# Optimization experiments

Measured on AMD Instinct MI355X. Metric: run time of the kernel, lower is better.

## Reference

```python
import jax, jax.numpy as jnp
import numpy as np

P, G, F, H = 128, 256, 1024, 512
EPS = 1e-5

def _bn(x, g, b, m, v):
    # eval-mode BatchNorm1d over last dim
    return (x - m) / jnp.sqrt(v + EPS) * g + b

def _lrelu(x):
    return jnp.where(x > 0, x, 0.1 * x)

def setup_inputs():
    key = jax.random.key(0)
    ks = iter(jax.random.split(key, 64))
    rn = lambda s, sc=1.0: jax.random.normal(next(ks), s, dtype=jnp.float32) * sc
    ru = lambda s: jax.random.uniform(next(ks), s, dtype=jnp.float32) + 0.5
    return {
        "f_p": rn((P, F)), "f_g": rn((G, F)),
        "bn_g": ru((F,)), "bn_b": rn((F,), 0.1), "bn_m": rn((F,), 0.1), "bn_v": ru((F,)),
        "rf_W1": rn((F, F), 0.02), "rf_b1": rn((F,), 0.01),
        "rf1_g": ru((F,)), "rf1_b": rn((F,), 0.1), "rf1_m": rn((F,), 0.1), "rf1_v": ru((F,)),
        "rf_W2": rn((F, F), 0.02), "rf_b2": rn((F,), 0.01),
        "rf2_g": ru((F,)), "rf2_b": rn((F,), 0.1), "rf2_m": rn((F,), 0.1), "rf2_v": ru((F,)),
        "sfc_W": rn((F, H), 0.02), "sfc_b": rn((H,), 0.01),
        "sbn_g": ru((H,)), "sbn_b": rn((H,), 0.1), "sbn_m": rn((H,), 0.1), "sbn_v": ru((H,)),
        "scl_W": rn((H, 1), 0.001), "scl_b": rn((1,), 0.001),
        "ffc_W": rn((F, H), 0.02), "ffc_b": rn((H,), 0.01),
        "fbn_g": ru((H,)), "fbn_b": rn((H,), 0.1), "fbn_m": rn((H,), 0.1), "fbn_v": ru((H,)),
        "cls_W": rn((H, 1), 0.001), "cls_b": rn((1,), 0.001),
    }

def reference(f_p, f_g, bn_g, bn_b, bn_m, bn_v,
              rf_W1, rf_b1, rf1_g, rf1_b, rf1_m, rf1_v,
              rf_W2, rf_b2, rf2_g, rf2_b, rf2_m, rf2_v,
              sfc_W, sfc_b, sbn_g, sbn_b, sbn_m, sbn_v, scl_W, scl_b,
              ffc_W, ffc_b, fbn_g, fbn_b, fbn_m, fbn_v, cls_W, cls_b):
    # Siamese difference feature for every probe-gallery pair: d [P,G,F]
    d = _bn((f_p[:, None, :] - f_g[None, :, :]) ** 2, bn_g, bn_b, bn_m, bn_v)
    h = _lrelu(_bn(d @ rf_W1 + rf_b1, rf1_g, rf1_b, rf1_m, rf1_v))
    t = _lrelu(_bn(h @ rf_W2 + rf_b2, rf2_g, rf2_b, rf2_m, rf2_v))
    # Gallery-gallery scalar affinities via Siamese FcBlock + ClassBlock: w [G,G]
    dg = _bn((f_g[:, None, :] - f_g[None, :, :]) ** 2, bn_g, bn_b, bn_m, bn_v)
    hg = _lrelu(_bn(dg @ sfc_W + sfc_b, sbn_g, sbn_b, sbn_m, sbn_v))
    w = (hg @ scl_W + scl_b)[..., 0]
    # Graph diffusion over the gallery axis: d_new = t @ w  [P,G,F]
    d_new = jnp.einsum('pgf,gh->phf', t, w)
    # Per-pair FC + classifier -> scalar score per (probe, gallery) pair
    feat = _lrelu(_bn(d_new @ ffc_W + ffc_b, fbn_g, fbn_b, fbn_m, fbn_v))
    result = (feat @ cls_W + cls_b)[..., 0]
    return result
```

## Files before the change

kernel.cpp:

```cpp
#include <hip/hip_runtime.h>


typedef __bf16 bf16;
typedef __attribute__((ext_vector_type(8))) __bf16 bf16x8;
typedef __attribute__((ext_vector_type(4))) float f32x4;

#define EPSV 1e-5f

__device__ __forceinline__ void async_load16(const bf16* g, bf16* l) {
    __builtin_amdgcn_global_load_lds(
        (const __attribute__((address_space(1))) void*)g,
        (__attribute__((address_space(3))) void*)l, 16, 0, 0);
}

__global__ __launch_bounds__(256) void prep_kernel(
    const float* __restrict__ g, const float* __restrict__ b,
    const float* __restrict__ m, const float* __restrict__ v,
    const float* __restrict__ bias, float* __restrict__ scale,
    float* __restrict__ offset, int n)
{
    int i = blockIdx.x * 256 + threadIdx.x;
    if (i >= n) return;
    float s = g[i] / sqrtf(v[i] + EPSV);
    float o = b[i] - m[i] * s;
    if (bias) o += bias[i] * s;
    scale[i] = s;
    offset[i] = o;
}

__global__ __launch_bounds__(256) void wtrans_kernel(
    const float* __restrict__ in, bf16* __restrict__ out, int K, int N)
{
    int k = blockIdx.x * 256 + threadIdx.x;
    int n = blockIdx.y;
    out[(size_t)n * K + k] = (bf16)in[(size_t)k * N + n];
}

__global__ __launch_bounds__(256) void wconv_kernel(
    const float* __restrict__ w_acc, const float* __restrict__ sclb,
    bf16* __restrict__ wT)
{
    int tid = blockIdx.x * 256 + threadIdx.x;
    int g2 = tid >> 8, g1 = tid & 255;
    int idx = ((g1 >> 4) <= (g2 >> 4)) ? (g1 * 256 + g2) : (g2 * 256 + g1);
    wT[tid] = (bf16)(w_acc[idx] + sclb[0]);
}

__global__ __launch_bounds__(256) void finout_kernel(
    const float* __restrict__ acc, const float* __restrict__ clsb,
    float* __restrict__ out)
{
    int i = blockIdx.x * 256 + threadIdx.x;
    out[i] = acc[i] + clsb[0];
}

__global__ __launch_bounds__(512) void gemm256(
    const bf16* __restrict__ A,
    const float* __restrict__ pairX, const float* __restrict__ pairY,
    const float* __restrict__ ps, const float* __restrict__ po,
    const bf16* __restrict__ BT,
    bf16* __restrict__ C,
    int K, int N, int rowOff,
    long long batchA, long long batchB, long long batchC,
    const float* __restrict__ scale, const float* __restrict__ offset,
    int lrelu,
    const float* __restrict__ fuseW, float* __restrict__ facc,
    long long faccStride)
{
    __shared__ bf16 As[256 * 64];
    __shared__ bf16 Bs[256 * 64];
    const int tid  = threadIdx.x;
    const int lane = tid & 63;
    const int wave = tid >> 6;
    const int wrow = wave >> 2, wcol = wave & 3;
    const int row0 = blockIdx.y * 256;
    const int col0 = blockIdx.x * 256;
    const int q = lane >> 4, l16 = lane & 15;
    const int z = blockIdx.z;

    const bf16* Ap = A + (size_t)z * (size_t)batchA;
    const bf16* Bp = BT + (size_t)z * (size_t)batchB;

    f32x4 acc[8][4];
#pragma unroll
    for (int mi = 0; mi < 8; ++mi)
#pragma unroll
        for (int ni = 0; ni < 4; ++ni)
#pragma unroll
            for (int e = 0; e < 4; ++e) acc[mi][ni][e] = 0.f;

    for (int kk = 0; kk < K; kk += 64) {
        if (pairX) {
#pragma unroll
            for (int t = 0; t < 4; ++t) {
                int c = tid + t * 512;
                int r = c >> 3, ch = c & 7;
                int gr = rowOff + row0 + r;
                const float* xp = pairX + (size_t)(gr >> 8) * K + kk + ch * 8;
                const float* yp = pairY + (size_t)(gr & 255) * K + kk + ch * 8;
                f32x4 x0 = *(const f32x4*)xp, x1 = *(const f32x4*)(xp + 4);
                f32x4 y0 = *(const f32x4*)yp, y1 = *(const f32x4*)(yp + 4);
                f32x4 sa = *(const f32x4*)(ps + kk + ch * 8);
                f32x4 sb = *(const f32x4*)(ps + kk + ch * 8 + 4);
                f32x4 oa = *(const f32x4*)(po + kk + ch * 8);
                f32x4 ob = *(const f32x4*)(po + kk + ch * 8 + 4);
                bf16x8 dv;
#pragma unroll
                for (int j = 0; j < 4; ++j) {
                    float d0 = x0[j] - y0[j];
                    float d1 = x1[j] - y1[j];
                    dv[j]     = (bf16)(d0 * d0 * sa[j] + oa[j]);
                    dv[j + 4] = (bf16)(d1 * d1 * sb[j] + ob[j]);
                }
                *(bf16x8*)&As[r * 64 + ((ch ^ (r & 7)) * 8)] = dv;
            }
        } else {
#pragma unroll
            for (int t = 0; t < 4; ++t) {
                int idx = t * 512 + tid;
                int r = idx >> 3, sch = idx & 7;
                int gch = sch ^ (r & 7);
                async_load16(Ap + (size_t)(row0 + r) * K + kk + gch * 8,
                             &As[idx * 8]);
            }
        }
#pragma unroll
        for (int t = 0; t < 4; ++t) {
            int idx = t * 512 + tid;
            int r = idx >> 3, sch = idx & 7;
            int gch = sch ^ (r & 7);
            async_load16(Bp + (size_t)(col0 + r) * K + kk + gch * 8,
                         &Bs[idx * 8]);
        }
        __syncthreads();

#pragma unroll
        for (int s = 0; s < 2; ++s) {
            bf16x8 af[8], bfr[4];
#pragma unroll
            for (int mi = 0; mi < 8; ++mi) {
                int r = wrow * 128 + mi * 16 + l16;
                af[mi] = *(const bf16x8*)&As[r * 64 + (((s * 4 + q) ^ (r & 7)) * 8)];
            }
#pragma unroll
            for (int ni = 0; ni < 4; ++ni) {
                int rc = wcol * 64 + ni * 16 + l16;
                bfr[ni] = *(const bf16x8*)&Bs[rc * 64 + (((s * 4 + q) ^ (rc & 7)) * 8)];
            }
#pragma unroll
            for (int mi = 0; mi < 8; ++mi)
#pragma unroll
                for (int ni = 0; ni < 4; ++ni)
                    acc[mi][ni] = __builtin_amdgcn_mfma_f32_16x16x32_bf16(
                        af[mi], bfr[ni], acc[mi][ni], 0, 0, 0);
        }
        __syncthreads();
    }

    if (fuseW) {
#pragma unroll
        for (int mi = 0; mi < 8; ++mi)
#pragma unroll
            for (int i = 0; i < 4; ++i) {
                float rs = 0.f;
#pragma unroll
                for (int ni = 0; ni < 4; ++ni) {
                    int cc = col0 + wcol * 64 + ni * 16 + l16;
                    float val = acc[mi][ni][i] * scale[cc] + offset[cc];
                    val = val > 0.f ? val : 0.1f * val;
                    rs += val * fuseW[cc];
                }
                rs += __shfl_xor(rs, 1, 64);
                rs += __shfl_xor(rs, 2, 64);
                rs += __shfl_xor(rs, 4, 64);
                rs += __shfl_xor(rs, 8, 64);
                if (l16 == 0) {
                    int r = row0 + wrow * 128 + mi * 16 + q * 4 + i;
                    atomicAdd(facc + (size_t)z * faccStride + r, rs);
                }
            }
        return;
    }
    bf16* Cp = C + (size_t)z * (size_t)batchC;
#pragma unroll
    for (int mi = 0; mi < 8; ++mi)
#pragma unroll
        for (int ni = 0; ni < 4; ++ni)
#pragma unroll
            for (int i = 0; i < 4; ++i) {
                int r = row0 + wrow * 128 + mi * 16 + q * 4 + i;
                int cc = col0 + wcol * 64 + ni * 16 + l16;
                float val = acc[mi][ni][i];
                if (scale) val = val * scale[cc] + offset[cc];
                if (lrelu) val = val > 0.f ? val : 0.1f * val;
                Cp[(size_t)r * N + cc] = (bf16)val;
            }
}

__global__ __launch_bounds__(512) void gemm_aff(
    const float* __restrict__ pairX,
    const float* __restrict__ ps, const float* __restrict__ po,
    const bf16* __restrict__ BT,
    int K,
    const float* __restrict__ scale, const float* __restrict__ offset,
    const float* __restrict__ sclW, float* __restrict__ w_acc)
{
    __shared__ bf16 As[256 * 64];
    __shared__ bf16 Bs[128 * 64];
    const int tid  = threadIdx.x;
    const int lane = tid & 63;
    const int wave = tid >> 6;
    const int wrow = wave >> 1, wcol = wave & 1;
    const int q = lane >> 4, l16 = lane & 15;
    const int col0 = blockIdx.x * 128;

    int ta = 0, rem = blockIdx.y;
    while (rem >= 16 - ta) { rem -= 16 - ta; ++ta; }
    const int tb = ta + rem;

    f32x4 acc[4][4];
#pragma unroll
    for (int mi = 0; mi < 4; ++mi)
#pragma unroll
        for (int ni = 0; ni < 4; ++ni)
#pragma unroll
            for (int e = 0; e < 4; ++e) acc[mi][ni][e] = 0.f;

    for (int kk = 0; kk < K; kk += 64) {
#pragma unroll
        for (int t = 0; t < 4; ++t) {
            int c = tid + t * 512;
            int r = c >> 3, ch = c & 7;
            int g1 = ta * 16 + (r >> 4), g2 = tb * 16 + (r & 15);
            const float* xp = pairX + (size_t)g1 * K + kk + ch * 8;
            const float* yp = pairX + (size_t)g2 * K + kk + ch * 8;
            f32x4 x0 = *(const f32x4*)xp, x1 = *(const f32x4*)(xp + 4);
            f32x4 y0 = *(const f32x4*)yp, y1 = *(const f32x4*)(yp + 4);
            f32x4 sa = *(const f32x4*)(ps + kk + ch * 8);
            f32x4 sb = *(const f32x4*)(ps + kk + ch * 8 + 4);
            f32x4 oa = *(const f32x4*)(po + kk + ch * 8);
            f32x4 ob = *(const f32x4*)(po + kk + ch * 8 + 4);
            bf16x8 dv;
#pragma unroll
            for (int j = 0; j < 4; ++j) {
                float d0 = x0[j] - y0[j];
                float d1 = x1[j] - y1[j];
                dv[j]     = (bf16)(d0 * d0 * sa[j] + oa[j]);
                dv[j + 4] = (bf16)(d1 * d1 * sb[j] + ob[j]);
            }
            *(bf16x8*)&As[r * 64 + ((ch ^ (r & 7)) * 8)] = dv;
        }
#pragma unroll
        for (int t = 0; t < 2; ++t) {
            int idx = t * 512 + tid;
            int r = idx >> 3, sch = idx & 7;
            int gch = sch ^ (r & 7);
            async_load16(BT + (size_t)(col0 + r) * K + kk + gch * 8,
                         &Bs[idx * 8]);
        }
        __syncthreads();

#pragma unroll
        for (int s = 0; s < 2; ++s) {
            bf16x8 af[4], bfr[4];
#pragma unroll
            for (int mi = 0; mi < 4; ++mi) {
                int r = wrow * 64 + mi * 16 + l16;
                af[mi] = *(const bf16x8*)&As[r * 64 + (((s * 4 + q) ^ (r & 7)) * 8)];
            }
#pragma unroll
            for (int ni = 0; ni < 4; ++ni) {
                int rc = wcol * 64 + ni * 16 + l16;
                bfr[ni] = *(const bf16x8*)&Bs[rc * 64 + (((s * 4 + q) ^ (rc & 7)) * 8)];
            }
#pragma unroll
            for (int mi = 0; mi < 4; ++mi)
#pragma unroll
                for (int ni = 0; ni < 4; ++ni)
                    acc[mi][ni] = __builtin_amdgcn_mfma_f32_16x16x32_bf16(
                        af[mi], bfr[ni], acc[mi][ni], 0, 0, 0);
        }
        __syncthreads();
    }

#pragma unroll
    for (int mi = 0; mi < 4; ++mi)
#pragma unroll
        for (int i = 0; i < 4; ++i) {
            float rs = 0.f;
#pragma unroll
            for (int ni = 0; ni < 4; ++ni) {
                int cc = col0 + wcol * 64 + ni * 16 + l16;
                float val = acc[mi][ni][i] * scale[cc] + offset[cc];
                val = val > 0.f ? val : 0.1f * val;
                rs += val * sclW[cc];
            }
            rs += __shfl_xor(rs, 1, 64);
            rs += __shfl_xor(rs, 2, 64);
            rs += __shfl_xor(rs, 4, 64);
            rs += __shfl_xor(rs, 8, 64);
            if (l16 == 0) {
                int r = wrow * 64 + mi * 16 + q * 4 + i;
                int g1 = ta * 16 + (r >> 4), g2 = tb * 16 + (r & 15);
                atomicAdd(w_acc + g1 * 256 + g2, rs);
            }
        }
}

extern "C" void kernel_launch(void* const* d_in, const int* in_sizes, int n_in,
                              void* d_out, int out_size, void* d_ws, size_t ws_size,
                              hipStream_t stream)
{
    const float* f_p   = (const float*)d_in[0];
    const float* f_g   = (const float*)d_in[1];
    const float* bn_g  = (const float*)d_in[2];
    const float* bn_b  = (const float*)d_in[3];
    const float* bn_m  = (const float*)d_in[4];
    const float* bn_v  = (const float*)d_in[5];
    const float* rf_W1 = (const float*)d_in[6];
    const float* rf_b1 = (const float*)d_in[7];
    const float* rf1_g = (const float*)d_in[8];
    const float* rf1_b = (const float*)d_in[9];
    const float* rf1_m = (const float*)d_in[10];
    const float* rf1_v = (const float*)d_in[11];
    const float* rf_W2 = (const float*)d_in[12];
    const float* rf_b2 = (const float*)d_in[13];
    const float* rf2_g = (const float*)d_in[14];
    const float* rf2_b = (const float*)d_in[15];
    const float* rf2_m = (const float*)d_in[16];
    const float* rf2_v = (const float*)d_in[17];
    const float* sfc_W = (const float*)d_in[18];
    const float* sfc_b = (const float*)d_in[19];
    const float* sbn_g = (const float*)d_in[20];
    const float* sbn_b = (const float*)d_in[21];
    const float* sbn_m = (const float*)d_in[22];
    const float* sbn_v = (const float*)d_in[23];
    const float* scl_W = (const float*)d_in[24];
    const float* scl_b = (const float*)d_in[25];
    const float* ffc_W = (const float*)d_in[26];
    const float* ffc_b = (const float*)d_in[27];
    const float* fbn_g = (const float*)d_in[28];
    const float* fbn_b = (const float*)d_in[29];
    const float* fbn_m = (const float*)d_in[30];
    const float* fbn_v = (const float*)d_in[31];
    const float* cls_W = (const float*)d_in[32];
    const float* cls_b = (const float*)d_in[33];

    const size_t MB = 1ull << 20;
    char* ws = (char*)d_ws;
    float* SC      = (float*)(ws);
    float *s0 = SC,        *o0 = SC + 1024;
    float *s1 = SC + 2048, *o1 = SC + 3072;
    float *s2 = SC + 4096, *o2 = SC + 5120;
    float *s3 = SC + 6144, *o3 = SC + 6656;
    float *s4 = SC + 7168, *o4 = SC + 7680;
    float* w_acc   = (float*)(ws + 65536);
    float* out_acc = (float*)(ws + 327680);
    bf16* wT       = (bf16*)(ws + 458752);
    bf16* W1T      = (bf16*)(ws + 1 * MB);
    bf16* W2T      = (bf16*)(ws + 3 * MB);
    bf16* sfcT     = (bf16*)(ws + 5 * MB);
    bf16* ffcT     = (bf16*)(ws + 6 * MB);

    int nc;
    if      (ws_size >= 170 * MB) nc = 1;
    else if (ws_size >= 90 * MB)  nc = 2;
    else                          nc = 4;
    const int pc = 128 / nc;
    const int R  = pc * 256;
    const size_t hbytes = (size_t)R * 1024 * 2;
    bf16* bufA = (bf16*)(ws + 8 * MB);
    bf16* bufB = (bf16*)(ws + 8 * MB + hbytes);
    bf16* bufC = (bf16*)(ws + 8 * MB + 2 * hbytes);

    prep_kernel<<<dim3(4), 256, 0, stream>>>(bn_g, bn_b, bn_m, bn_v, nullptr, s0, o0, 1024);
    prep_kernel<<<dim3(4), 256, 0, stream>>>(rf1_g, rf1_b, rf1_m, rf1_v, rf_b1, s1, o1, 1024);
    prep_kernel<<<dim3(4), 256, 0, stream>>>(rf2_g, rf2_b, rf2_m, rf2_v, rf_b2, s2, o2, 1024);
    prep_kernel<<<dim3(2), 256, 0, stream>>>(sbn_g, sbn_b, sbn_m, sbn_v, sfc_b, s3, o3, 512);
    prep_kernel<<<dim3(2), 256, 0, stream>>>(fbn_g, fbn_b, fbn_m, fbn_v, ffc_b, s4, o4, 512);

    wtrans_kernel<<<dim3(4, 1024), 256, 0, stream>>>(rf_W1, W1T, 1024, 1024);
    wtrans_kernel<<<dim3(4, 1024), 256, 0, stream>>>(rf_W2, W2T, 1024, 1024);
    wtrans_kernel<<<dim3(4, 512), 256, 0, stream>>>(sfc_W, sfcT, 1024, 512);
    wtrans_kernel<<<dim3(4, 512), 256, 0, stream>>>(ffc_W, ffcT, 1024, 512);

    hipMemsetAsync(ws + 65536, 0, 393216, stream);

    gemm_aff<<<dim3(4, 136), 512, 0, stream>>>(
        f_g, s0, o0, sfcT, 1024, s3, o3, scl_W, w_acc);
    wconv_kernel<<<dim3(256), 256, 0, stream>>>(w_acc, scl_b, wT);

    for (int ci = 0; ci < nc; ++ci) {
        gemm256<<<dim3(4, R / 256), 512, 0, stream>>>(
            nullptr, f_p, f_g, s0, o0, W1T, bufA, 1024, 1024, ci * R,
            0, 0, 0, s1, o1, 1, nullptr, nullptr, 0);
        gemm256<<<dim3(4, R / 256), 512, 0, stream>>>(
            bufA, nullptr, nullptr, nullptr, nullptr, W2T, bufB, 1024, 1024, 0,
            0, 0, 0, s2, o2, 1, nullptr, nullptr, 0);
        gemm256<<<dim3(1, 2, pc), 512, 0, stream>>>(
            ffcT, nullptr, nullptr, nullptr, nullptr, bufB, bufC, 1024, 256, 0,
            0, (long long)256 * 1024, (long long)512 * 256,
            nullptr, nullptr, 0, nullptr, nullptr, 0);
        gemm256<<<dim3(2, 1, pc), 512, 0, stream>>>(
            wT, nullptr, nullptr, nullptr, nullptr, bufC, nullptr, 256, 512, 0,
            0, (long long)512 * 256, 0,
            s4, o4, 1, cls_W, out_acc + (size_t)ci * pc * 256, 256);
    }
    finout_kernel<<<dim3(128), 256, 0, stream>>>(out_acc, cls_b, (float*)d_out);
}
```

Measured before the change: 566.7 us.

## Fuse gallery affinity GEMM into second ReFine GEMM launch as extra blocks

Adds a combined kernel whose first blocks compute the second ReFine linear layer and whose remaining blocks compute the gallery-gallery affinity GEMM with its fused classifier reduction. This lets the small affinity work fill the GPU alongside the large GEMM instead of running as a separate serial launch beforehand. The combined path is used only when the whole pair set fits in one chunk. Mixing heterogeneous blocks may unbalance scheduling, and the shared memory footprint is sized for the larger tile.

```diff
diff --git a/kernel.cpp b/kernel.cpp
--- a/kernel.cpp
+++ b/kernel.cpp
@@ -52,6 +52,214 @@
 {
     int i = blockIdx.x * 256 + threadIdx.x;
     out[i] = acc[i] + clsb[0];
+}
+
+__device__ __forceinline__ void dev_gemm256_plain(
+    bf16* As, bf16* Bs,
+    const bf16* __restrict__ A, const bf16* __restrict__ BT,
+    bf16* __restrict__ C, int K, int N, int row0, int col0,
+    const float* __restrict__ scale, const float* __restrict__ offset,
+    int lrelu)
+{
+    const int tid  = threadIdx.x;
+    const int lane = tid & 63;
+    const int wave = tid >> 6;
+    const int wrow = wave >> 2, wcol = wave & 3;
+    const int q = lane >> 4, l16 = lane & 15;
+
+    f32x4 acc[8][4];
+#pragma unroll
+    for (int mi = 0; mi < 8; ++mi)
+#pragma unroll
+        for (int ni = 0; ni < 4; ++ni)
+#pragma unroll
+            for (int e = 0; e < 4; ++e) acc[mi][ni][e] = 0.f;
+
+    for (int kk = 0; kk < K; kk += 64) {
+#pragma unroll
+        for (int t = 0; t < 4; ++t) {
+            int idx = t * 512 + tid;
+            int r = idx >> 3, sch = idx & 7;
+            int gch = sch ^ (r & 7);
+            async_load16(A + (size_t)(row0 + r) * K + kk + gch * 8,
+                         &As[idx * 8]);
+        }
+#pragma unroll
+        for (int t = 0; t < 4; ++t) {
+            int idx = t * 512 + tid;
+            int r = idx >> 3, sch = idx & 7;
+            int gch = sch ^ (r & 7);
+            async_load16(BT + (size_t)(col0 + r) * K + kk + gch * 8,
+                         &Bs[idx * 8]);
+        }
+        __syncthreads();
+#pragma unroll
+        for (int s = 0; s < 2; ++s) {
+            bf16x8 af[8], bfr[4];
+#pragma unroll
+            for (int mi = 0; mi < 8; ++mi) {
+                int r = wrow * 128 + mi * 16 + l16;
+                af[mi] = *(const bf16x8*)&As[r * 64 + (((s * 4 + q) ^ (r & 7)) * 8)];
+            }
+#pragma unroll
+            for (int ni = 0; ni < 4; ++ni) {
+                int rc = wcol * 64 + ni * 16 + l16;
+                bfr[ni] = *(const bf16x8*)&Bs[rc * 64 + (((s * 4 + q) ^ (rc & 7)) * 8)];
+            }
+#pragma unroll
+            for (int mi = 0; mi < 8; ++mi)
+#pragma unroll
+                for (int ni = 0; ni < 4; ++ni)
+                    acc[mi][ni] = __builtin_amdgcn_mfma_f32_16x16x32_bf16(
+                        af[mi], bfr[ni], acc[mi][ni], 0, 0, 0);
+        }
+        __syncthreads();
+    }
+
+#pragma unroll
+    for (int mi = 0; mi < 8; ++mi)
+#pragma unroll
+        for (int ni = 0; ni < 4; ++ni)
+#pragma unroll
+            for (int i = 0; i < 4; ++i) {
+                int r = row0 + wrow * 128 + mi * 16 + q * 4 + i;
+                int cc = col0 + wcol * 64 + ni * 16 + l16;
+                float val = acc[mi][ni][i];
+                if (scale) val = val * scale[cc] + offset[cc];
+                if (lrelu) val = val > 0.f ? val : 0.1f * val;
+                C[(size_t)r * N + cc] = (bf16)val;
+            }
+}
+
+__device__ __forceinline__ void dev_aff(
+    bf16* As, bf16* Bs,
+    const float* __restrict__ pairX,
+    const float* __restrict__ ps, const float* __restrict__ po,
+    const bf16* __restrict__ BT, int K, int col0, int triIdx,
+    const float* __restrict__ scale, const float* __restrict__ offset,
+    const float* __restrict__ sclW, float* __restrict__ w_acc)
+{
+    const int tid  = threadIdx.x;
+    const int lane = tid & 63;
+    const int wave = tid >> 6;
+    const int wrow = wave >> 1, wcol = wave & 1;
+    const int q = lane >> 4, l16 = lane & 15;
+
+    int ta = 0, rem = triIdx;
+    while (rem >= 16 - ta) { rem -= 16 - ta; ++ta; }
+    const int tb = ta + rem;
+
+    f32x4 acc[4][4];
+#pragma unroll
+    for (int mi = 0; mi < 4; ++mi)
+#pragma unroll
+        for (int ni = 0; ni < 4; ++ni)
+#pragma unroll
+            for (int e = 0; e < 4; ++e) acc[mi][ni][e] = 0.f;
+
+    for (int kk = 0; kk < K; kk += 64) {
+#pragma unroll
+        for (int t = 0; t < 4; ++t) {
+            int c = tid + t * 512;
+            int r = c >> 3, ch = c & 7;
+            int g1 = ta * 16 + (r >> 4), g2 = tb * 16 + (r & 15);
+            const float* xp = pairX + (size_t)g1 * K + kk + ch * 8;
+            const float* yp = pairX + (size_t)g2 * K + kk + ch * 8;
+            f32x4 x0 = *(const f32x4*)xp, x1 = *(const f32x4*)(xp + 4);
+            f32x4 y0 = *(const f32x4*)yp, y1 = *(const f32x4*)(yp + 4);
+            f32x4 sa = *(const f32x4*)(ps + kk + ch * 8);
+            f32x4 sb = *(const f32x4*)(ps + kk + ch * 8 + 4);
+            f32x4 oa = *(const f32x4*)(po + kk + ch * 8);
+            f32x4 ob = *(const f32x4*)(po + kk + ch * 8 + 4);
+            bf16x8 dv;
+#pragma unroll
+            for (int j = 0; j < 4; ++j) {
+                float d0 = x0[j] - y0[j];
+                float d1 = x1[j] - y1[j];
+                dv[j]     = (bf16)(d0 * d0 * sa[j] + oa[j]);
+                dv[j + 4] = (bf16)(d1 * d1 * sb[j] + ob[j]);
+            }
+            *(bf16x8*)&As[r * 64 + ((ch ^ (r & 7)) * 8)] = dv;
+        }
+#pragma unroll
+        for (int t = 0; t < 2; ++t) {
+            int idx = t * 512 + tid;
+            int r = idx >> 3, sch = idx & 7;
+            int gch = sch ^ (r & 7);
+            async_load16(BT + (size_t)(col0 + r) * K + kk + gch * 8,
+                         &Bs[idx * 8]);
+        }
+        __syncthreads();
+
+#pragma unroll
+        for (int s = 0; s < 2; ++s) {
+            bf16x8 af[4], bfr[4];
+#pragma unroll
+            for (int mi = 0; mi < 4; ++mi) {
+                int r = wrow * 64 + mi * 16 + l16;
+                af[mi] = *(const bf16x8*)&As[r * 64 + (((s * 4 + q) ^ (r & 7)) * 8)];
+            }
+#pragma unroll
+            for (int ni = 0; ni < 4; ++ni) {
+                int rc = wcol * 64 + ni * 16 + l16;
+                bfr[ni] = *(const bf16x8*)&Bs[rc * 64 + (((s * 4 + q) ^ (rc & 7)) * 8)];
+            }
+#pragma unroll
+            for (int mi = 0; mi < 4; ++mi)
+#pragma unroll
+                for (int ni = 0; ni < 4; ++ni)
+                    acc[mi][ni] = __builtin_amdgcn_mfma_f32_16x16x32_bf16(
+                        af[mi], bfr[ni], acc[mi][ni], 0, 0, 0);
+        }
+        __syncthreads();
+    }
+
+#pragma unroll
+    for (int mi = 0; mi < 4; ++mi)
+#pragma unroll
+        for (int i = 0; i < 4; ++i) {
+            float rs = 0.f;
+#pragma unroll
+            for (int ni = 0; ni < 4; ++ni) {
+                int cc = col0 + wcol * 64 + ni * 16 + l16;
+                float val = acc[mi][ni][i] * scale[cc] + offset[cc];
+                val = val > 0.f ? val : 0.1f * val;
+                rs += val * sclW[cc];
+            }
+            rs += __shfl_xor(rs, 1, 64);
+            rs += __shfl_xor(rs, 2, 64);
+            rs += __shfl_xor(rs, 4, 64);
+            rs += __shfl_xor(rs, 8, 64);
+            if (l16 == 0) {
+                int r = wrow * 64 + mi * 16 + q * 4 + i;
+                int g1 = ta * 16 + (r >> 4), g2 = tb * 16 + (r & 15);
+                atomicAdd(w_acc + g1 * 256 + g2, rs);
+            }
+        }
+}
+
+__global__ __launch_bounds__(512) void gemm_taff(
+    const bf16* __restrict__ hbuf, const bf16* __restrict__ W2T,
+    bf16* __restrict__ tbuf,
+    const float* __restrict__ s2, const float* __restrict__ o2,
+    const float* __restrict__ f_g,
+    const float* __restrict__ ps0, const float* __restrict__ po0,
+    const bf16* __restrict__ sfcT,
+    const float* __restrict__ s3, const float* __restrict__ o3,
+    const float* __restrict__ sclW, float* __restrict__ w_acc,
+    int tBlocks)
+{
+    __shared__ bf16 As[256 * 64];
+    __shared__ bf16 Bs[256 * 64];
+    int b = blockIdx.x;
+    if (b < tBlocks) {
+        dev_gemm256_plain(As, Bs, hbuf, W2T, tbuf, 1024, 1024,
+                          (b >> 2) * 256, (b & 3) * 256, s2, o2, 1);
+    } else {
+        int b2 = b - tBlocks;
+        dev_aff(As, Bs, f_g, ps0, po0, sfcT, 1024,
+                (b2 & 3) * 128, b2 >> 2, s3, o3, sclW, w_acc);
+    }
 }
 
 __global__ __launch_bounds__(512) void gemm256(
@@ -200,111 +408,14 @@
 __global__ __launch_bounds__(512) void gemm_aff(
     const float* __restrict__ pairX,
     const float* __restrict__ ps, const float* __restrict__ po,
-    const bf16* __restrict__ BT,
-    int K,
+    const bf16* __restrict__ BT, int K,
     const float* __restrict__ scale, const float* __restrict__ offset,
     const float* __restrict__ sclW, float* __restrict__ w_acc)
 {
     __shared__ bf16 As[256 * 64];
     __shared__ bf16 Bs[128 * 64];
-    const int tid  = threadIdx.x;
-    const int lane = tid & 63;
-    const int wave = tid >> 6;
-    const int wrow = wave >> 1, wcol = wave & 1;
-    const int q = lane >> 4, l16 = lane & 15;
-    const int col0 = blockIdx.x * 128;
-
-    int ta = 0, rem = blockIdx.y;
-    while (rem >= 16 - ta) { rem -= 16 - ta; ++ta; }
-    const int tb = ta + rem;
-
-    f32x4 acc[4][4];
-#pragma unroll
-    for (int mi = 0; mi < 4; ++mi)
-#pragma unroll
-        for (int ni = 0; ni < 4; ++ni)
-#pragma unroll
-            for (int e = 0; e < 4; ++e) acc[mi][ni][e] = 0.f;
-
-    for (int kk = 0; kk < K; kk += 64) {
-#pragma unroll
-        for (int t = 0; t < 4; ++t) {
-            int c = tid + t * 512;
-            int r = c >> 3, ch = c & 7;
-            int g1 = ta * 16 + (r >> 4), g2 = tb * 16 + (r & 15);
-            const float* xp = pairX + (size_t)g1 * K + kk + ch * 8;
-            const float* yp = pairX + (size_t)g2 * K + kk + ch * 8;
-            f32x4 x0 = *(const f32x4*)xp, x1 = *(const f32x4*)(xp + 4);
-            f32x4 y0 = *(const f32x4*)yp, y1 = *(const f32x4*)(yp + 4);
-            f32x4 sa = *(const f32x4*)(ps + kk + ch * 8);
-            f32x4 sb = *(const f32x4*)(ps + kk + ch * 8 + 4);
-            f32x4 oa = *(const f32x4*)(po + kk + ch * 8);
-            f32x4 ob = *(const f32x4*)(po + kk + ch * 8 + 4);
-            bf16x8 dv;
-#pragma unroll
-            for (int j = 0; j < 4; ++j) {
-                float d0 = x0[j] - y0[j];
-                float d1 = x1[j] - y1[j];
-                dv[j]     = (bf16)(d0 * d0 * sa[j] + oa[j]);
-                dv[j + 4] = (bf16)(d1 * d1 * sb[j] + ob[j]);
-            }
-            *(bf16x8*)&As[r * 64 + ((ch ^ (r & 7)) * 8)] = dv;
-        }
-#pragma unroll
-        for (int t = 0; t < 2; ++t) {
-            int idx = t * 512 + tid;
-            int r = idx >> 3, sch = idx & 7;
-            int gch = sch ^ (r & 7);
-            async_load16(BT + (size_t)(col0 + r) * K + kk + gch * 8,
-                         &Bs[idx * 8]);
-        }
-        __syncthreads();
-
-#pragma unroll
-        for (int s = 0; s < 2; ++s) {
-            bf16x8 af[4], bfr[4];
-#pragma unroll
-            for (int mi = 0; mi < 4; ++mi) {
-                int r = wrow * 64 + mi * 16 + l16;
-                af[mi] = *(const bf16x8*)&As[r * 64 + (((s * 4 + q) ^ (r & 7)) * 8)];
-            }
-#pragma unroll
-            for (int ni = 0; ni < 4; ++ni) {
-                int rc = wcol * 64 + ni * 16 + l16;
-                bfr[ni] = *(const bf16x8*)&Bs[rc * 64 + (((s * 4 + q) ^ (rc & 7)) * 8)];
-            }
-#pragma unroll
-            for (int mi = 0; mi < 4; ++mi)
-#pragma unroll
-                for (int ni = 0; ni < 4; ++ni)
-                    acc[mi][ni] = __builtin_amdgcn_mfma_f32_16x16x32_bf16(
-                        af[mi], bfr[ni], acc[mi][ni], 0, 0, 0);
-        }
-        __syncthreads();
-    }
-
-#pragma unroll
-    for (int mi = 0; mi < 4; ++mi)
-#pragma unroll
-        for (int i = 0; i < 4; ++i) {
-            float rs = 0.f;
-#pragma unroll
-            for (int ni = 0; ni < 4; ++ni) {
-                int cc = col0 + wcol * 64 + ni * 16 + l16;
-                float val = acc[mi][ni][i] * scale[cc] + offset[cc];
-                val = val > 0.f ? val : 0.1f * val;
-                rs += val * sclW[cc];
-            }
-            rs += __shfl_xor(rs, 1, 64);
-            rs += __shfl_xor(rs, 2, 64);
-            rs += __shfl_xor(rs, 4, 64);
-            rs += __shfl_xor(rs, 8, 64);
-            if (l16 == 0) {
-                int r = wrow * 64 + mi * 16 + q * 4 + i;
-                int g1 = ta * 16 + (r >> 4), g2 = tb * 16 + (r & 15);
-                atomicAdd(w_acc + g1 * 256 + g2, rs);
-            }
-        }
+    dev_aff(As, Bs, pairX, ps, po, BT, K,
+            blockIdx.x * 128, blockIdx.y, scale, offset, sclW, w_acc);
 }
 
 extern "C" void kernel_launch(void* const* d_in, const int* in_sizes, int n_in,
@@ -386,25 +497,42 @@
 
     hipMemsetAsync(ws + 65536, 0, 393216, stream);
 
-    gemm_aff<<<dim3(4, 136), 512, 0, stream>>>(
-        f_g, s0, o0, sfcT, 1024, s3, o3, scl_W, w_acc);
-    wconv_kernel<<<dim3(256), 256, 0, stream>>>(w_acc, scl_b, wT);
-
-    for (int ci = 0; ci < nc; ++ci) {
-        gemm256<<<dim3(4, R / 256), 512, 0, stream>>>(
-            nullptr, f_p, f_g, s0, o0, W1T, bufA, 1024, 1024, ci * R,
+    if (nc == 1) {
+        gemm256<<<dim3(4, 128), 512, 0, stream>>>(
+            nullptr, f_p, f_g, s0, o0, W1T, bufA, 1024, 1024, 0,
             0, 0, 0, s1, o1, 1, nullptr, nullptr, 0);
-        gemm256<<<dim3(4, R / 256), 512, 0, stream>>>(
-            bufA, nullptr, nullptr, nullptr, nullptr, W2T, bufB, 1024, 1024, 0,
-            0, 0, 0, s2, o2, 1, nullptr, nullptr, 0);
-        gemm256<<<dim3(1, 2, pc), 512, 0, stream>>>(
+        gemm_taff<<<dim3(512 + 544), 512, 0, stream>>>(
+            bufA, W2T, bufB, s2, o2,
+            f_g, s0, o0, sfcT, s3, o3, scl_W, w_acc, 512);
+        wconv_kernel<<<dim3(256), 256, 0, stream>>>(w_acc, scl_b, wT);
+        gemm256<<<dim3(1, 2, 128), 512, 0, stream>>>(
             ffcT, nullptr, nullptr, nullptr, nullptr, bufB, bufC, 1024, 256, 0,
             0, (long long)256 * 1024, (long long)512 * 256,
             nullptr, nullptr, 0, nullptr, nullptr, 0);
-        gemm256<<<dim3(2, 1, pc), 512, 0, stream>>>(
+        gemm256<<<dim3(2, 1, 128), 512, 0, stream>>>(
             wT, nullptr, nullptr, nullptr, nullptr, bufC, nullptr, 256, 512, 0,
             0, (long long)512 * 256, 0,
-            s4, o4, 1, cls_W, out_acc + (size_t)ci * pc * 256, 256);
+            s4, o4, 1, cls_W, out_acc, 256);
+    } else {
+        gemm_aff<<<dim3(4, 136), 512, 0, stream>>>(
+            f_g, s0, o0, sfcT, 1024, s3, o3, scl_W, w_acc);
+        wconv_kernel<<<dim3(256), 256, 0, stream>>>(w_acc, scl_b, wT);
+        for (int ci = 0; ci < nc; ++ci) {
+            gemm256<<<dim3(4, R / 256), 512, 0, stream>>>(
+                nullptr, f_p, f_g, s0, o0, W1T, bufA, 1024, 1024, ci * R,
+                0, 0, 0, s1, o1, 1, nullptr, nullptr, 0);
+            gemm256<<<dim3(4, R / 256), 512, 0, stream>>>(
+                bufA, nullptr, nullptr, nullptr, nullptr, W2T, bufB, 1024, 1024, 0,
+                0, 0, 0, s2, o2, 1, nullptr, nullptr, 0);
+            gemm256<<<dim3(1, 2, pc), 512, 0, stream>>>(
+                ffcT, nullptr, nullptr, nullptr, nullptr, bufB, bufC, 1024, 256, 0,
+                0, (long long)256 * 1024, (long long)512 * 256,
+                nullptr, nullptr, 0, nullptr, nullptr, 0);
+            gemm256<<<dim3(2, 1, pc), 512, 0, stream>>>(
+                wT, nullptr, nullptr, nullptr, nullptr, bufC, nullptr, 256, 512, 0,
+                0, (long long)512 * 256, 0,
+                s4, o4, 1, cls_W, out_acc + (size_t)ci * pc * 256, 256);
+        }
     }
     finout_kernel<<<dim3(128), 256, 0, stream>>>(out_acc, cls_b, (float*)d_out);
 }
```

After: 575.4 us. Within noise of the previous version (+1.5%).
